# Performance work log

Measured on AMD Instinct MI355X. Metric: run time of the kernel, lower is better.

The kernel has to match this reference:

```python
import jax, jax.numpy as jnp
import numpy as np

N, T, V, F = 32, 5, 64, 512

def setup_inputs() -> dict:
    key = jax.random.key(0)
    k1, k2 = jax.random.split(key)
    x = jax.random.normal(k1, (N, T, V, F), dtype=jnp.float32)
    # keras 'uniform' initializer ~ U(-0.05, 0.05)
    a = jax.random.uniform(k2, (F, 1), dtype=jnp.float32, minval=-0.05, maxval=0.05)
    return {"x": x, "a": a}

def reference(x, a):
    # x: (N, T, V, F); take middle time slice -> (N, V, F)
    t_mid = x.shape[1] // 2
    xm = x[:, t_mid, :, :]
    # diff[n, i, j, f] = x[n, i, f] - x[n, j, f]  (matches the TF broadcast+transpose,
    # reordered so batch is leading; the later perm=[1,0,2,3] did the same reorder)
    absdiff = jnp.abs(xm[:, :, None, :] - xm[:, None, :, :])  # (N, V, V, F)
    # learned linear reduce over F, then exp -> unnormalized scores (N, V, V)
    tmpS = jnp.exp(jnp.einsum('nijf,f->nij', absdiff, a[:, 0]))
    # TF normalization: S[n,i,j] = tmpS[n,i,j] / sum_k tmpS[n,k,i]
    colsum = jnp.sum(tmpS, axis=1)  # (N, V), indexed [n, i]
    S = tmpS / colsum[:, :, None]
    return S
```

## Files before the change

kernel.cpp:

```cpp
#include <hip/hip_runtime.h>
#include <hip/hip_bf16.h>


#define NN 32
#define TT 5
#define VV 64
#define FF 512
#define TMID 2
#define IB 4

__global__ __launch_bounds__(256) void pairsim_kernel(
    const float* __restrict__ x, const float* __restrict__ a,
    float* __restrict__ out) {
  const int b = blockIdx.x;
  const int n = b >> 4;
  const int i0 = (b & 15) * IB;
  const int t = threadIdx.x;

  __shared__ float xi[IB * FF];
  __shared__ float av[FF];
  __shared__ float red[IB][VV];

  const float* xm = x + ((size_t)n * TT + TMID) * (size_t)VV * FF;

  {
    const float4* src_xi = reinterpret_cast<const float4*>(xm + (size_t)i0 * FF);
    const float4* src_a  = reinterpret_cast<const float4*>(a);
    float4* dst_xi = reinterpret_cast<float4*>(xi);
    float4* dst_a  = reinterpret_cast<float4*>(av);
    for (int idx = t; idx < (IB * FF / 4) + (FF / 4); idx += 256) {
      if (idx < IB * FF / 4) dst_xi[idx] = src_xi[idx];
      else                   dst_a[idx - IB * FF / 4] = src_a[idx - IB * FF / 4];
    }
  }
  __syncthreads();

  const int j = t >> 2;
  const int part = t & 3;
  const float* xj = xm + (size_t)j * FF;

  float acc0 = 0.f, acc1 = 0.f, acc2 = 0.f, acc3 = 0.f;
#pragma unroll
  for (int k = 0; k < 32; ++k) {
    const int f = k * 16 + part * 4;
    float4 vj = *reinterpret_cast<const float4*>(xj + f);
    float4 va = *reinterpret_cast<const float4*>(av + f);
    float4 v0 = *reinterpret_cast<const float4*>(xi + 0 * FF + f);
    float4 v1 = *reinterpret_cast<const float4*>(xi + 1 * FF + f);
    float4 v2 = *reinterpret_cast<const float4*>(xi + 2 * FF + f);
    float4 v3 = *reinterpret_cast<const float4*>(xi + 3 * FF + f);
    acc0 = fmaf(fabsf(v0.x - vj.x), va.x, acc0);
    acc0 = fmaf(fabsf(v0.y - vj.y), va.y, acc0);
    acc0 = fmaf(fabsf(v0.z - vj.z), va.z, acc0);
    acc0 = fmaf(fabsf(v0.w - vj.w), va.w, acc0);
    acc1 = fmaf(fabsf(v1.x - vj.x), va.x, acc1);
    acc1 = fmaf(fabsf(v1.y - vj.y), va.y, acc1);
    acc1 = fmaf(fabsf(v1.z - vj.z), va.z, acc1);
    acc1 = fmaf(fabsf(v1.w - vj.w), va.w, acc1);
    acc2 = fmaf(fabsf(v2.x - vj.x), va.x, acc2);
    acc2 = fmaf(fabsf(v2.y - vj.y), va.y, acc2);
    acc2 = fmaf(fabsf(v2.z - vj.z), va.z, acc2);
    acc2 = fmaf(fabsf(v2.w - vj.w), va.w, acc2);
    acc3 = fmaf(fabsf(v3.x - vj.x), va.x, acc3);
    acc3 = fmaf(fabsf(v3.y - vj.y), va.y, acc3);
    acc3 = fmaf(fabsf(v3.z - vj.z), va.z, acc3);
    acc3 = fmaf(fabsf(v3.w - vj.w), va.w, acc3);
  }
  acc0 += __shfl_xor(acc0, 1); acc0 += __shfl_xor(acc0, 2);
  acc1 += __shfl_xor(acc1, 1); acc1 += __shfl_xor(acc1, 2);
  acc2 += __shfl_xor(acc2, 1); acc2 += __shfl_xor(acc2, 2);
  acc3 += __shfl_xor(acc3, 1); acc3 += __shfl_xor(acc3, 2);

  if (part == 0) {
    red[0][j] = expf(acc0);
    red[1][j] = expf(acc1);
    red[2][j] = expf(acc2);
    red[3][j] = expf(acc3);
  }
  __syncthreads();

  {
    const int w = t >> 6;
    const int lane = t & 63;
    float v = red[w][lane];
    float s = v;
#pragma unroll
    for (int o = 1; o < 64; o <<= 1) s += __shfl_xor(s, o);
    out[(((size_t)n * VV + i0 + w) << 6) + lane] = v / s;
  }
}

extern "C" void kernel_launch(void* const* d_in, const int* in_sizes, int n_in,
                              void* d_out, int out_size, void* d_ws, size_t ws_size,
                              hipStream_t stream) {
  const float* x = (const float*)d_in[0];
  const float* a = (const float*)d_in[1];
  float* out = (float*)d_out;
  pairsim_kernel<<<NN * (VV / IB), 256, 0, stream>>>(x, a, out);
}
```

Before: 11.98 us.

## Register-tile 4x4 i/j pairs per thread with prefetched x_j loads

Each thread now accumulates a 4x4 block of (i,j) pairs across 16 feature lanes instead of 4 i values for a single j. This reuses the shared-memory x_i and a reads across four j rows and cuts LDS traffic per FMA. The global x_j loads for the first chunk are issued before the barrier, and each later chunk is software-prefetched one iteration ahead in a non-unrolled loop. In exchange it adds a 4-step shuffle reduction for all 16 accumulators, a select chain to pick each thread's value, and a padded reduction buffer, with higher register pressure.

```diff
diff --git a/kernel.cpp b/kernel.cpp
--- a/kernel.cpp
+++ b/kernel.cpp
@@ -8,6 +8,7 @@
 #define FF 512
 #define TMID 2
 #define IB 4
+#define RSTRIDE 65
 
 __global__ __launch_bounds__(256) void pairsim_kernel(
     const float* __restrict__ x, const float* __restrict__ a,
@@ -19,7 +20,7 @@
 
   __shared__ float xi[IB * FF];
   __shared__ float av[FF];
-  __shared__ float red[IB][VV];
+  __shared__ float red[IB * RSTRIDE];
 
   const float* xm = x + ((size_t)n * TT + TMID) * (size_t)VV * FF;
 
@@ -33,56 +34,97 @@
       else                   dst_a[idx - IB * FF / 4] = src_a[idx - IB * FF / 4];
     }
   }
+
+  const int part = t & 15;
+  const int jg   = t >> 4;
+  const float* xj0 = xm + (size_t)(jg     ) * FF;
+  const float* xj1 = xm + (size_t)(jg + 16) * FF;
+  const float* xj2 = xm + (size_t)(jg + 32) * FF;
+  const float* xj3 = xm + (size_t)(jg + 48) * FF;
+
+  float acc[4][4];
+#pragma unroll
+  for (int i = 0; i < 4; ++i)
+#pragma unroll
+    for (int js = 0; js < 4; ++js) acc[i][js] = 0.f;
+
+  int f = part * 4;
+  float4 vj0 = *reinterpret_cast<const float4*>(xj0 + f);
+  float4 vj1 = *reinterpret_cast<const float4*>(xj1 + f);
+  float4 vj2 = *reinterpret_cast<const float4*>(xj2 + f);
+  float4 vj3 = *reinterpret_cast<const float4*>(xj3 + f);
+
   __syncthreads();
 
-  const int j = t >> 2;
-  const int part = t & 3;
-  const float* xj = xm + (size_t)j * FF;
+#pragma unroll 1
+  for (int k = 0; k < 8; ++k) {
+    const int fn = (k + 1) * 64 + part * 4;
+    float4 nj0, nj1, nj2, nj3;
+    if (k < 7) {
+      nj0 = *reinterpret_cast<const float4*>(xj0 + fn);
+      nj1 = *reinterpret_cast<const float4*>(xj1 + fn);
+      nj2 = *reinterpret_cast<const float4*>(xj2 + fn);
+      nj3 = *reinterpret_cast<const float4*>(xj3 + fn);
+    }
+    const int fc = k * 64 + part * 4;
+    float4 va = *reinterpret_cast<const float4*>(av + fc);
+    float4 vi[4];
+    vi[0] = *reinterpret_cast<const float4*>(xi + 0 * FF + fc);
+    vi[1] = *reinterpret_cast<const float4*>(xi + 1 * FF + fc);
+    vi[2] = *reinterpret_cast<const float4*>(xi + 2 * FF + fc);
+    vi[3] = *reinterpret_cast<const float4*>(xi + 3 * FF + fc);
 
-  float acc0 = 0.f, acc1 = 0.f, acc2 = 0.f, acc3 = 0.f;
 #pragma unroll
-  for (int k = 0; k < 32; ++k) {
-    const int f = k * 16 + part * 4;
-    float4 vj = *reinterpret_cast<const float4*>(xj + f);
-    float4 va = *reinterpret_cast<const float4*>(av + f);
-    float4 v0 = *reinterpret_cast<const float4*>(xi + 0 * FF + f);
-    float4 v1 = *reinterpret_cast<const float4*>(xi + 1 * FF + f);
-    float4 v2 = *reinterpret_cast<const float4*>(xi + 2 * FF + f);
-    float4 v3 = *reinterpret_cast<const float4*>(xi + 3 * FF + f);
-    acc0 = fmaf(fabsf(v0.x - vj.x), va.x, acc0);
-    acc0 = fmaf(fabsf(v0.y - vj.y), va.y, acc0);
-    acc0 = fmaf(fabsf(v0.z - vj.z), va.z, acc0);
-    acc0 = fmaf(fabsf(v0.w - vj.w), va.w, acc0);
-    acc1 = fmaf(fabsf(v1.x - vj.x), va.x, acc1);
-    acc1 = fmaf(fabsf(v1.y - vj.y), va.y, acc1);
-    acc1 = fmaf(fabsf(v1.z - vj.z), va.z, acc1);
-    acc1 = fmaf(fabsf(v1.w - vj.w), va.w, acc1);
-    acc2 = fmaf(fabsf(v2.x - vj.x), va.x, acc2);
-    acc2 = fmaf(fabsf(v2.y - vj.y), va.y, acc2);
-    acc2 = fmaf(fabsf(v2.z - vj.z), va.z, acc2);
-    acc2 = fmaf(fabsf(v2.w - vj.w), va.w, acc2);
-    acc3 = fmaf(fabsf(v3.x - vj.x), va.x, acc3);
-    acc3 = fmaf(fabsf(v3.y - vj.y), va.y, acc3);
-    acc3 = fmaf(fabsf(v3.z - vj.z), va.z, acc3);
-    acc3 = fmaf(fabsf(v3.w - vj.w), va.w, acc3);
+    for (int i = 0; i < 4; ++i) {
+      acc[i][0] = fmaf(fabsf(vi[i].x - vj0.x), va.x, acc[i][0]);
+      acc[i][0] = fmaf(fabsf(vi[i].y - vj0.y), va.y, acc[i][0]);
+      acc[i][0] = fmaf(fabsf(vi[i].z - vj0.z), va.z, acc[i][0]);
+      acc[i][0] = fmaf(fabsf(vi[i].w - vj0.w), va.w, acc[i][0]);
+      acc[i][1] = fmaf(fabsf(vi[i].x - vj1.x), va.x, acc[i][1]);
+      acc[i][1] = fmaf(fabsf(vi[i].y - vj1.y), va.y, acc[i][1]);
+      acc[i][1] = fmaf(fabsf(vi[i].z - vj1.z), va.z, acc[i][1]);
+      acc[i][1] = fmaf(fabsf(vi[i].w - vj1.w), va.w, acc[i][1]);
+      acc[i][2] = fmaf(fabsf(vi[i].x - vj2.x), va.x, acc[i][2]);
+      acc[i][2] = fmaf(fabsf(vi[i].y - vj2.y), va.y, acc[i][2]);
+      acc[i][2] = fmaf(fabsf(vi[i].z - vj2.z), va.z, acc[i][2]);
+      acc[i][2] = fmaf(fabsf(vi[i].w - vj2.w), va.w, acc[i][2]);
+      acc[i][3] = fmaf(fabsf(vi[i].x - vj3.x), va.x, acc[i][3]);
+      acc[i][3] = fmaf(fabsf(vi[i].y - vj3.y), va.y, acc[i][3]);
+      acc[i][3] = fmaf(fabsf(vi[i].z - vj3.z), va.z, acc[i][3]);
+      acc[i][3] = fmaf(fabsf(vi[i].w - vj3.w), va.w, acc[i][3]);
+    }
+    vj0 = nj0; vj1 = nj1; vj2 = nj2; vj3 = nj3;
   }
-  acc0 += __shfl_xor(acc0, 1); acc0 += __shfl_xor(acc0, 2);
-  acc1 += __shfl_xor(acc1, 1); acc1 += __shfl_xor(acc1, 2);
-  acc2 += __shfl_xor(acc2, 1); acc2 += __shfl_xor(acc2, 2);
-  acc3 += __shfl_xor(acc3, 1); acc3 += __shfl_xor(acc3, 2);
 
-  if (part == 0) {
-    red[0][j] = expf(acc0);
-    red[1][j] = expf(acc1);
-    red[2][j] = expf(acc2);
-    red[3][j] = expf(acc3);
+#pragma unroll
+  for (int i = 0; i < 4; ++i)
+#pragma unroll
+    for (int js = 0; js < 4; ++js) {
+      float v = acc[i][js];
+      v += __shfl_xor(v, 1);
+      v += __shfl_xor(v, 2);
+      v += __shfl_xor(v, 4);
+      v += __shfl_xor(v, 8);
+      acc[i][js] = v;
+    }
+
+  {
+    const int ri = part & 3;
+    const int rj = part >> 2;
+    float pick = 0.f;
+#pragma unroll
+    for (int i = 0; i < 4; ++i)
+#pragma unroll
+      for (int js = 0; js < 4; ++js)
+        if (ri == i && rj == js) pick = acc[i][js];
+    red[ri * RSTRIDE + jg + (rj << 4)] = expf(pick);
   }
   __syncthreads();
 
   {
     const int w = t >> 6;
     const int lane = t & 63;
-    float v = red[w][lane];
+    float v = red[w * RSTRIDE + lane];
     float s = v;
 #pragma unroll
     for (int o = 1; o < 64; o <<= 1) s += __shfl_xor(s, o);
```

After: 14.57 us. 21.6% more time.
